# Kernel optimization log

Hardware: AMD Instinct MI355X
Metric: run time of the kernel (lower is better)

## Reference

```python
import jax, jax.numpy as jnp
import numpy as np

N_KNOTS = 4
OUT_DIM = 512
IN_DIM = 512
BATCH = 4096


def setup_inputs() -> dict:
    key = jax.random.key(0)
    k1, k2, k3 = jax.random.split(key, 3)
    # inputs: [B, IN_DIM + N_KNOTS]; last N_KNOTS cols are phase blend weights
    x = jax.random.normal(k1, (BATCH, IN_DIM + N_KNOTS), dtype=jnp.float32)
    # make the phase columns a valid convex-ish blend (softmax), as in PFNN usage
    phase = jax.nn.softmax(x[:, -N_KNOTS:], axis=-1)
    x = jnp.concatenate([x[:, :-N_KNOTS], phase], axis=-1)
    bound = np.sqrt(6.0 / (OUT_DIM * IN_DIM))
    weight_knots = jax.random.uniform(k2, (N_KNOTS, OUT_DIM, IN_DIM), dtype=jnp.float32,
                                      minval=-bound, maxval=bound)
    bias_knots = jnp.zeros((N_KNOTS, OUT_DIM), dtype=jnp.float32)
    return {"inputs": x, "weight_knots": weight_knots, "bias_knots": bias_knots}


def reference(inputs, weight_knots, bias_knots):
    # Split features and phase blend coefficients
    p = inputs[:, -N_KNOTS:]          # [B, K]
    feat = inputs[:, :-N_KNOTS]       # [B, IN]
    # Original: wi = sum_k p[:,k] * W[k]  ([B,out,in]); res = wi @ feat + bi.
    # Fused equivalent: contract W with feat first, then blend over knots,
    # avoiding the [B,out,in] intermediate.
    # knot_out: [B, K, OUT]
    knot_out = jnp.einsum('koi,bi->bko', weight_knots, feat)
    res = jnp.einsum('bk,bko->bo', p, knot_out) + p @ bias_knots  # [B, OUT]
    res = jax.nn.elu(res)
    return res
```

## Files before the change

### kernel.cpp

```cpp
#include <hip/hip_runtime.h>

#define BATCH 4096
#define IN_DIM 512
#define OUT_DIM 512
#define NK 4
#define SX (IN_DIM + NK)
#define BM 64
#define BN 32
#define BK 64

typedef short bf16x8 __attribute__((ext_vector_type(8)));
typedef float f32x4 __attribute__((ext_vector_type(4)));

__device__ __forceinline__ unsigned short f2bf(float f) {
    unsigned int u = __float_as_uint(f);
    u = u + 0x7FFFu + ((u >> 16) & 1u);
    return (unsigned short)(u >> 16);
}

__device__ __forceinline__ void gload_lds16(const void* g, void* l) {
    __builtin_amdgcn_global_load_lds(
        (const __attribute__((address_space(1))) void*)g,
        (__attribute__((address_space(3))) void*)l, 16, 0, 0);
}

__global__ __launch_bounds__(256) void convert_kernel(
    const float* __restrict__ x, const float* __restrict__ w,
    unsigned short* __restrict__ wb, unsigned short* __restrict__ fb)
{
    const int WCH = NK * OUT_DIM * IN_DIM / 4;
    int g = blockIdx.x * 256 + threadIdx.x;
    if (g < WCH) {
        const float4 v = reinterpret_cast<const float4*>(w)[g];
        unsigned short h[4] = {f2bf(v.x), f2bf(v.y), f2bf(v.z), f2bf(v.w)};
        *reinterpret_cast<uint2*>(&wb[g * 4]) = *reinterpret_cast<const uint2*>(h);
    } else {
        int idx = g - WCH;
        int row = idx >> 7;
        int c   = (idx & 127) * 4;
        const float4 v = *reinterpret_cast<const float4*>(&x[(size_t)row * SX + c]);
        unsigned short h[4] = {f2bf(v.x), f2bf(v.y), f2bf(v.z), f2bf(v.w)};
        *reinterpret_cast<uint2*>(&fb[row * IN_DIM + c]) = *reinterpret_cast<const uint2*>(h);
    }
}

__global__ __launch_bounds__(128) void mpl_gemm(
    const unsigned short* __restrict__ fb,
    const unsigned short* __restrict__ wb,
    const float* __restrict__ x,
    const float* __restrict__ bias,
    float* __restrict__ out)
{
    __shared__ unsigned short As[BM * BK];
    __shared__ unsigned short Bs[NK * BN * BK];

    const int tid  = threadIdx.x;
    const int lane = tid & 63;
    const int wid  = tid >> 6;
    const int wr   = wid * 32;
    const int R0   = blockIdx.x * BM;
    const int C0   = blockIdx.y * BN;

    f32x4 acc[NK][2][2] = {};
    const int cl = lane & 15;
    const int kb = (lane >> 4) * 8;

    for (int kt = 0; kt < IN_DIM / BK; ++kt) {
        const int k0 = kt * BK;
        __syncthreads();
        #pragma unroll
        for (int j = 0; j < 4; ++j) {
            int ch  = j * 128 + tid;
            int row = ch >> 3;
            int c   = ch & 7;
            gload_lds16(fb + (size_t)(R0 + row) * IN_DIM + k0 + ((c ^ (row & 7)) << 3),
                        &As[ch * 8]);
        }
        #pragma unroll
        for (int j = 0; j < 8; ++j) {
            int ch  = j * 128 + tid;
            int kn  = ch >> 8;
            int rem = ch & 255;
            int row = rem >> 3;
            int c   = rem & 7;
            gload_lds16(wb + (size_t)kn * OUT_DIM * IN_DIM + (size_t)(C0 + row) * IN_DIM
                           + k0 + ((c ^ (row & 7)) << 3),
                        &Bs[kn * BN * BK + (rem << 3)]);
        }
        __syncthreads();
        __builtin_amdgcn_s_setprio(1);
        #pragma unroll
        for (int kk = 0; kk < BK; kk += 32) {
            bf16x8 af[2];
            #pragma unroll
            for (int m = 0; m < 2; ++m) {
                int row  = wr + m * 16 + cl;
                int boff = (row * 128 + (kk + kb) * 2) ^ ((row & 7) << 4);
                af[m] = *reinterpret_cast<const bf16x8*>(
                    reinterpret_cast<const char*>(As) + boff);
            }
            #pragma unroll
            for (int kn = 0; kn < NK; ++kn) {
                bf16x8 bfr[2];
                #pragma unroll
                for (int n = 0; n < 2; ++n) {
                    int row  = n * 16 + cl;
                    int boff = (row * 128 + (kk + kb) * 2) ^ ((row & 7) << 4);
                    bfr[n] = *reinterpret_cast<const bf16x8*>(
                        reinterpret_cast<const char*>(Bs) + kn * (BN * BK * 2) + boff);
                }
                #pragma unroll
                for (int m = 0; m < 2; ++m)
                    #pragma unroll
                    for (int n = 0; n < 2; ++n)
                        acc[kn][m][n] = __builtin_amdgcn_mfma_f32_16x16x32_bf16(
                            af[m], bfr[n], acc[kn][m][n], 0, 0, 0);
            }
        }
        __builtin_amdgcn_s_setprio(0);
    }

    const int rl = (lane >> 4) * 4;
    float bcol[2][NK];
    #pragma unroll
    for (int n = 0; n < 2; ++n)
        #pragma unroll
        for (int k = 0; k < NK; ++k)
            bcol[n][k] = bias[k * OUT_DIM + C0 + n * 16 + cl];

    #pragma unroll
    for (int m = 0; m < 2; ++m) {
        #pragma unroll
        for (int r = 0; r < 4; ++r) {
            const int row = R0 + wr + m * 16 + rl + r;
            const float4 p = *reinterpret_cast<const float4*>(&x[(size_t)row * SX + IN_DIM]);
            const float pk[4] = {p.x, p.y, p.z, p.w};
            #pragma unroll
            for (int n = 0; n < 2; ++n) {
                float v = 0.f;
                #pragma unroll
                for (int k = 0; k < NK; ++k)
                    v += pk[k] * (acc[k][m][n][r] + bcol[n][k]);
                v = (v > 0.f) ? v : expm1f(v);
                out[(size_t)row * OUT_DIM + C0 + n * 16 + cl] = v;
            }
        }
    }
}

#define LDT 72
__global__ __launch_bounds__(256) void mpl_kernel_fb(
    const float* __restrict__ x, const float* __restrict__ w,
    const float* __restrict__ bias, float* __restrict__ out)
{
    __shared__ unsigned short Asf[BM][LDT];
    __shared__ unsigned short Bsf[NK][64][LDT];
    const int tid = threadIdx.x, lane = tid & 63, wid = tid >> 6;
    const int wr = (wid >> 1) * 32, wc = (wid & 1) * 32;
    const int R0 = blockIdx.x * BM, C0 = blockIdx.y * 64;
    f32x4 acc[NK][2][2] = {};
    const int cl = lane & 15, kb = (lane >> 4) * 8;
    for (int kt = 0; kt < IN_DIM / BK; ++kt) {
        const int k0 = kt * BK;
        __syncthreads();
        #pragma unroll
        for (int j = 0; j < 4; ++j) {
            int f = tid + 256 * j, row = f >> 4, c4 = (f & 15) * 4;
            const float4 v = *reinterpret_cast<const float4*>(&x[(size_t)(R0 + row) * SX + k0 + c4]);
            unsigned short h[4] = {f2bf(v.x), f2bf(v.y), f2bf(v.z), f2bf(v.w)};
            *reinterpret_cast<uint2*>(&Asf[row][c4]) = *reinterpret_cast<const uint2*>(h);
        }
        #pragma unroll
        for (int kn = 0; kn < NK; ++kn)
            #pragma unroll
            for (int j = 0; j < 4; ++j) {
                int f = tid + 256 * j, row = f >> 4, c4 = (f & 15) * 4;
                const float4 v = *reinterpret_cast<const float4*>(
                    &w[(size_t)kn * OUT_DIM * IN_DIM + (size_t)(C0 + row) * IN_DIM + k0 + c4]);
                unsigned short h[4] = {f2bf(v.x), f2bf(v.y), f2bf(v.z), f2bf(v.w)};
                *reinterpret_cast<uint2*>(&Bsf[kn][row][c4]) = *reinterpret_cast<const uint2*>(h);
            }
        __syncthreads();
        #pragma unroll
        for (int kk = 0; kk < BK; kk += 32) {
            bf16x8 af[2];
            #pragma unroll
            for (int m = 0; m < 2; ++m)
                af[m] = *reinterpret_cast<const bf16x8*>(&Asf[wr + m * 16 + cl][kk + kb]);
            #pragma unroll
            for (int kn = 0; kn < NK; ++kn) {
                bf16x8 bfr[2];
                #pragma unroll
                for (int n = 0; n < 2; ++n)
                    bfr[n] = *reinterpret_cast<const bf16x8*>(&Bsf[kn][wc + n * 16 + cl][kk + kb]);
                #pragma unroll
                for (int m = 0; m < 2; ++m)
                    #pragma unroll
                    for (int n = 0; n < 2; ++n)
                        acc[kn][m][n] = __builtin_amdgcn_mfma_f32_16x16x32_bf16(
                            af[m], bfr[n], acc[kn][m][n], 0, 0, 0);
            }
        }
    }
    const int rl = (lane >> 4) * 4;
    float bcol[2][NK];
    #pragma unroll
    for (int n = 0; n < 2; ++n)
        #pragma unroll
        for (int k = 0; k < NK; ++k)
            bcol[n][k] = bias[k * OUT_DIM + C0 + wc + n * 16 + cl];
    #pragma unroll
    for (int m = 0; m < 2; ++m)
        #pragma unroll
        for (int r = 0; r < 4; ++r) {
            const int row = R0 + wr + m * 16 + rl + r;
            const float4 p = *reinterpret_cast<const float4*>(&x[(size_t)row * SX + IN_DIM]);
            const float pk[4] = {p.x, p.y, p.z, p.w};
            #pragma unroll
            for (int n = 0; n < 2; ++n) {
                float v = 0.f;
                #pragma unroll
                for (int k = 0; k < NK; ++k)
                    v += pk[k] * (acc[k][m][n][r] + bcol[n][k]);
                v = (v > 0.f) ? v : expm1f(v);
                out[(size_t)row * OUT_DIM + C0 + wc + n * 16 + cl] = v;
            }
        }
}

extern "C" void kernel_launch(void* const* d_in, const int* in_sizes, int n_in,
                              void* d_out, int out_size, void* d_ws, size_t ws_size,
                              hipStream_t stream) {
    const float* x    = (const float*)d_in[0];
    const float* w    = (const float*)d_in[1];
    const float* bias = (const float*)d_in[2];
    float* out        = (float*)d_out;

    const size_t wb_bytes = (size_t)NK * OUT_DIM * IN_DIM * 2;
    const size_t fb_bytes = (size_t)BATCH * IN_DIM * 2;

    if (ws_size < wb_bytes + fb_bytes) {
        dim3 grid(BATCH / BM, OUT_DIM / 64);
        mpl_kernel_fb<<<grid, dim3(256), 0, stream>>>(x, w, bias, out);
        return;
    }

    unsigned short* wb = (unsigned short*)d_ws;
    unsigned short* fb = (unsigned short*)((char*)d_ws + wb_bytes);

    const int total_chunks = NK * OUT_DIM * IN_DIM / 4 + BATCH * IN_DIM / 4;
    convert_kernel<<<dim3(total_chunks / 256), dim3(256), 0, stream>>>(x, w, wb, fb);

    dim3 grid(BATCH / BM, OUT_DIM / BN);
    mpl_gemm<<<grid, dim3(128), 0, stream>>>(fb, wb, x, bias, out);
}
```

Before: 27.19 us.

## Keep full-K weight panel in LDS and stream activations directly from global

The GEMM kernel now loads the whole 4-knot x 32-column x 512-K bf16 weight panel (128 KB) into LDS once, with a swizzle, and uses 512-thread blocks that each cover 256 batch rows. The per-K-tile barrier loop and the LDS staging of activations are gone; A fragments are read straight from global memory inside a fully unrolled K loop. This removes the repeated barriers and global-to-LDS copies of the weights. In exchange, the large LDS footprint limits how many blocks fit per CU, and the uncoalesced, unstaged global loads of A may stall the MFMA pipeline. The grid becomes 16x16 = 256 blocks.

```diff
diff --git a/kernel.cpp b/kernel.cpp
--- a/kernel.cpp
+++ b/kernel.cpp
@@ -5,9 +5,8 @@
 #define OUT_DIM 512
 #define NK 4
 #define SX (IN_DIM + NK)
-#define BM 64
-#define BN 32
-#define BK 64
+#define BMR 256
+#define BNC 32
 
 typedef short bf16x8 __attribute__((ext_vector_type(8)));
 typedef float f32x4 __attribute__((ext_vector_type(4)));
@@ -44,80 +43,66 @@
     }
 }
 
-__global__ __launch_bounds__(128) void mpl_gemm(
+__global__ __launch_bounds__(512, 2) void mpl_gemm(
     const unsigned short* __restrict__ fb,
     const unsigned short* __restrict__ wb,
     const float* __restrict__ x,
     const float* __restrict__ bias,
     float* __restrict__ out)
 {
-    __shared__ unsigned short As[BM * BK];
-    __shared__ unsigned short Bs[NK * BN * BK];
+    __shared__ unsigned short Bs[NK * BNC * IN_DIM];
 
     const int tid  = threadIdx.x;
     const int lane = tid & 63;
     const int wid  = tid >> 6;
     const int wr   = wid * 32;
-    const int R0   = blockIdx.x * BM;
-    const int C0   = blockIdx.y * BN;
+    const int R0   = blockIdx.x * BMR;
+    const int C0   = blockIdx.y * BNC;
+
+    #pragma unroll
+    for (int j = 0; j < 16; ++j) {
+        int ch  = j * 512 + tid;
+        int gr  = ch >> 6;
+        int c   = ch & 63;
+        int kn  = gr >> 5;
+        int col = gr & 31;
+        gload_lds16(wb + (size_t)kn * OUT_DIM * IN_DIM + (size_t)(C0 + col) * IN_DIM
+                       + ((c ^ (col & 7)) << 3),
+                    &Bs[ch * 8]);
+    }
+    __syncthreads();
 
     f32x4 acc[NK][2][2] = {};
     const int cl = lane & 15;
     const int kb = (lane >> 4) * 8;
 
-    for (int kt = 0; kt < IN_DIM / BK; ++kt) {
-        const int k0 = kt * BK;
-        __syncthreads();
-        #pragma unroll
-        for (int j = 0; j < 4; ++j) {
-            int ch  = j * 128 + tid;
-            int row = ch >> 3;
-            int c   = ch & 7;
-            gload_lds16(fb + (size_t)(R0 + row) * IN_DIM + k0 + ((c ^ (row & 7)) << 3),
-                        &As[ch * 8]);
-        }
-        #pragma unroll
-        for (int j = 0; j < 8; ++j) {
-            int ch  = j * 128 + tid;
-            int kn  = ch >> 8;
-            int rem = ch & 255;
-            int row = rem >> 3;
-            int c   = rem & 7;
-            gload_lds16(wb + (size_t)kn * OUT_DIM * IN_DIM + (size_t)(C0 + row) * IN_DIM
-                           + k0 + ((c ^ (row & 7)) << 3),
-                        &Bs[kn * BN * BK + (rem << 3)]);
-        }
-        __syncthreads();
-        __builtin_amdgcn_s_setprio(1);
-        #pragma unroll
-        for (int kk = 0; kk < BK; kk += 32) {
-            bf16x8 af[2];
-            #pragma unroll
-            for (int m = 0; m < 2; ++m) {
-                int row  = wr + m * 16 + cl;
-                int boff = (row * 128 + (kk + kb) * 2) ^ ((row & 7) << 4);
-                af[m] = *reinterpret_cast<const bf16x8*>(
-                    reinterpret_cast<const char*>(As) + boff);
-            }
-            #pragma unroll
-            for (int kn = 0; kn < NK; ++kn) {
-                bf16x8 bfr[2];
-                #pragma unroll
-                for (int n = 0; n < 2; ++n) {
-                    int row  = n * 16 + cl;
-                    int boff = (row * 128 + (kk + kb) * 2) ^ ((row & 7) << 4);
-                    bfr[n] = *reinterpret_cast<const bf16x8*>(
-                        reinterpret_cast<const char*>(Bs) + kn * (BN * BK * 2) + boff);
-                }
-                #pragma unroll
-                for (int m = 0; m < 2; ++m)
-                    #pragma unroll
-                    for (int n = 0; n < 2; ++n)
-                        acc[kn][m][n] = __builtin_amdgcn_mfma_f32_16x16x32_bf16(
-                            af[m], bfr[n], acc[kn][m][n], 0, 0, 0);
-            }
-        }
-        __builtin_amdgcn_s_setprio(0);
+    #pragma unroll
+    for (int kx = 0; kx < IN_DIM / 32; ++kx) {
+        const int k0 = kx * 32;
+        bf16x8 af[2];
+        #pragma unroll
+        for (int m = 0; m < 2; ++m)
+            af[m] = *reinterpret_cast<const bf16x8*>(
+                &fb[(size_t)(R0 + wr + m * 16 + cl) * IN_DIM + k0 + kb]);
+        #pragma unroll
+        for (int kn = 0; kn < NK; ++kn) {
+            bf16x8 bfr[2];
+            #pragma unroll
+            for (int n = 0; n < 2; ++n) {
+                int col  = n * 16 + cl;
+                int boff = (((kn * BNC + col) * IN_DIM + k0 + kb) * 2) ^ ((col & 7) << 4);
+                bfr[n] = *reinterpret_cast<const bf16x8*>(
+                    reinterpret_cast<const char*>(Bs) + boff);
+            }
+            __builtin_amdgcn_s_setprio(1);
+            #pragma unroll
+            for (int m = 0; m < 2; ++m)
+                #pragma unroll
+                for (int n = 0; n < 2; ++n)
+                    acc[kn][m][n] = __builtin_amdgcn_mfma_f32_16x16x32_bf16(
+                        af[m], bfr[n], acc[kn][m][n], 0, 0, 0);
+            __builtin_amdgcn_s_setprio(0);
+        }
     }
 
     const int rl = (lane >> 4) * 4;
@@ -153,15 +138,15 @@
     const float* __restrict__ x, const float* __restrict__ w,
     const float* __restrict__ bias, float* __restrict__ out)
 {
-    __shared__ unsigned short Asf[BM][LDT];
+    __shared__ unsigned short Asf[64][LDT];
     __shared__ unsigned short Bsf[NK][64][LDT];
     const int tid = threadIdx.x, lane = tid & 63, wid = tid >> 6;
     const int wr = (wid >> 1) * 32, wc = (wid & 1) * 32;
-    const int R0 = blockIdx.x * BM, C0 = blockIdx.y * 64;
+    const int R0 = blockIdx.x * 64, C0 = blockIdx.y * 64;
     f32x4 acc[NK][2][2] = {};
     const int cl = lane & 15, kb = (lane >> 4) * 8;
-    for (int kt = 0; kt < IN_DIM / BK; ++kt) {
-        const int k0 = kt * BK;
+    for (int kt = 0; kt < IN_DIM / 64; ++kt) {
+        const int k0 = kt * 64;
         __syncthreads();
         #pragma unroll
         for (int j = 0; j < 4; ++j) {
@@ -182,7 +167,7 @@
             }
         __syncthreads();
         #pragma unroll
-        for (int kk = 0; kk < BK; kk += 32) {
+        for (int kk = 0; kk < 64; kk += 32) {
             bf16x8 af[2];
             #pragma unroll
             for (int m = 0; m < 2; ++m)
@@ -240,7 +225,7 @@
     const size_t fb_bytes = (size_t)BATCH * IN_DIM * 2;
 
     if (ws_size < wb_bytes + fb_bytes) {
-        dim3 grid(BATCH / BM, OUT_DIM / 64);
+        dim3 grid(BATCH / 64, OUT_DIM / 64);
         mpl_kernel_fb<<<grid, dim3(256), 0, stream>>>(x, w, bias, out);
         return;
     }
@@ -251,6 +236,6 @@
     const int total_chunks = NK * OUT_DIM * IN_DIM / 4 + BATCH * IN_DIM / 4;
     convert_kernel<<<dim3(total_chunks / 256), dim3(256), 0, stream>>>(x, w, wb, fb);
 
-    dim3 grid(BATCH / BM, OUT_DIM / BN);
-    mpl_gemm<<<grid, dim3(128), 0, stream>>>(fb, wb, x, bias, out);
-}
+    dim3 grid(BATCH / BMR, OUT_DIM / BNC);
+    mpl_gemm<<<grid, dim3(512), 0, stream>>>(fb, wb, x, bias, out);
+}
```

Result: slower. 29.72 us (+9.3%).
